# Kernel tuning notes

Measured on AMD Instinct MI355X. Metric: run time of the kernel, lower is better.

The kernel has to match this reference:

```python
import jax, jax.numpy as jnp
import numpy as np

B, C, H, W = 16, 64, 64, 64

def setup_inputs() -> dict:
    key = jax.random.key(0)
    k1, k2, k3, k4, k5 = jax.random.split(key, 5)
    x = jax.random.normal(k1, (B, C, H, W), dtype=jnp.float32)
    w1 = jax.random.normal(k2, (C // 2, C), dtype=jnp.float32) * (1.0 / np.sqrt(C))
    w2 = jax.random.normal(k3, (C // 2, C), dtype=jnp.float32) * (1.0 / np.sqrt(C))
    w3 = jax.random.normal(k4, (C, C), dtype=jnp.float32) * (1.0 / np.sqrt(C))
    gamma = jax.random.normal(k5, (1,), dtype=jnp.float32)
    return {"x": x, "w1": w1, "w2": w2, "w3": w3, "gamma": gamma}

def reference(x, w1, w2, w3, gamma):
    b, c, h, w = x.shape
    n = h * w
    xf = x.reshape(b, c, n)                      # [B, C, N] (1x1 conv == channel matmul)
    c1 = jnp.einsum('dc,bcn->bdn', w1, xf)       # [B, C/2, N]
    c2 = jnp.einsum('dc,bcn->bdn', w2, xf)       # [B, C/2, N]
    c3 = jnp.einsum('oc,bcn->bon', w3, xf)       # [B, C, N]
    # matrix[b,i,j] = sum_d c2[b,d,i] * c1[b,d,j]
    matrix = jnp.einsum('bdi,bdj->bij', c2, c1)  # [B, N, N]
    attention = jax.nn.softmax(matrix, axis=-1)  # softmax over last dim
    # refined[b,c,k] = sum_j c3[b,c,j] * attention[b,k,j]
    refined = jnp.einsum('bcj,bkj->bck', c3, attention)  # [B, C, N]
    refined = refined.reshape(b, c, h, w)
    return gamma[0] * refined + x
```

## Files before the change

kernel.cpp:

```cpp
#include <hip/hip_runtime.h>
#include <hip/hip_bf16.h>

#define Bn 16
#define Nn 4096
#define LOG2E 1.44269504088896f

#if __has_builtin(__builtin_amdgcn_exp2f)
#define EXP2(x) __builtin_amdgcn_exp2f(x)
#else
#define EXP2(x) __expf((x) * 0.69314718055994531f)
#endif

typedef __attribute__((ext_vector_type(8))) short bf16x8;
typedef __attribute__((ext_vector_type(16))) float f32x16;

static __device__ __forceinline__ unsigned short f2bf(float f) {
    union { float f; unsigned int u; } v; v.f = f;
    return (unsigned short)((v.u + 0x7fffu + ((v.u >> 16) & 1u)) >> 16);
}
static __device__ __forceinline__ int cvtpk(float lo, float hi) {
    int d; asm("v_cvt_pk_bf16_f32 %0, %1, %2" : "=v"(d) : "v"(lo), "v"(hi)); return d;
}
static __device__ __forceinline__ bf16x8 mkfrag(int a, int b, int c, int d) {
    union { int i[4]; bf16x8 v; } u; u.i[0]=a; u.i[1]=b; u.i[2]=c; u.i[3]=d; return u.v;
}

__global__ __launch_bounds__(256) void qkv_kernel(
    const float* __restrict__ x,
    const float* __restrict__ w1,
    const float* __restrict__ w2,
    const float* __restrict__ w3,
    uint4* __restrict__ Qf,
    uint4* __restrict__ Kf,
    uint4* __restrict__ Vf)
{
    __shared__ float wlds[128 * 64];
    __shared__ __align__(16) unsigned short vtile[64][136];

    const int t = threadIdx.x;
    {
        float4* wd = (float4*)wlds;
        const float4* s1 = (const float4*)w1;
        const float4* s2 = (const float4*)w2;
        const float4* s3 = (const float4*)w3;
        wd[t]       = s1[t];
        wd[256 + t] = s1[256 + t];
        wd[512 + t] = s2[t];
        wd[768 + t] = s2[256 + t];
        #pragma unroll
        for (int k = 0; k < 4; ++k) wd[1024 + k * 256 + t] = s3[k * 256 + t];
    }

    const int half = t >> 7;
    const int nl = t & 127;
    const int b = blockIdx.x >> 5;
    const int n = ((blockIdx.x & 31) << 7) + nl;
    const float* xb = x + ((size_t)b << 18) + n;
    float xr[64];
    #pragma unroll
    for (int c = 0; c < 64; ++c) xr[c] = xb[(size_t)c << 12];

    __syncthreads();

    if (half == 0) {
        const int ntile = ((blockIdx.x & 31) << 2) + (nl >> 5);
        #pragma unroll
        for (int sel = 0; sel < 2; ++sel) {
            const float* wbase = wlds + sel * 2048;
            const float scl = sel ? 1.0f : LOG2E;
            uint4* dst = (sel ? Qf : Kf) + (((size_t)b * 128 + ntile) * 2) * 64;
            #pragma unroll
            for (int dt = 0; dt < 2; ++dt) {
                float acc[16];
                #pragma unroll
                for (int i = 0; i < 16; ++i) {
                    const float* wr = wbase + (dt * 16 + i) * 64;
                    float a = 0.f;
                    #pragma unroll
                    for (int c4 = 0; c4 < 16; ++c4) {
                        const float4 wv = *(const float4*)(wr + c4 * 4);
                        a = fmaf(wv.x, xr[c4 * 4 + 0], a);
                        a = fmaf(wv.y, xr[c4 * 4 + 1], a);
                        a = fmaf(wv.z, xr[c4 * 4 + 2], a);
                        a = fmaf(wv.w, xr[c4 * 4 + 3], a);
                    }
                    acc[i] = a * scl;
                }
                uint4 u0, u1;
                u0.x = (unsigned)f2bf(acc[0])  | ((unsigned)f2bf(acc[1])  << 16);
                u0.y = (unsigned)f2bf(acc[2])  | ((unsigned)f2bf(acc[3])  << 16);
                u0.z = (unsigned)f2bf(acc[4])  | ((unsigned)f2bf(acc[5])  << 16);
                u0.w = (unsigned)f2bf(acc[6])  | ((unsigned)f2bf(acc[7])  << 16);
                u1.x = (unsigned)f2bf(acc[8])  | ((unsigned)f2bf(acc[9])  << 16);
                u1.y = (unsigned)f2bf(acc[10]) | ((unsigned)f2bf(acc[11]) << 16);
                u1.z = (unsigned)f2bf(acc[12]) | ((unsigned)f2bf(acc[13]) << 16);
                u1.w = (unsigned)f2bf(acc[14]) | ((unsigned)f2bf(acc[15]) << 16);
                dst[(size_t)dt * 64 + (nl & 31)]      = u0;
                dst[(size_t)dt * 64 + 32 + (nl & 31)] = u1;
            }
        }
    } else {
        #pragma unroll
        for (int dg = 0; dg < 8; ++dg) {
            #pragma unroll
            for (int i = 0; i < 8; ++i) {
                const float* wr = wlds + (64 + dg * 8 + i) * 64;
                float a = 0.f;
                #pragma unroll
                for (int c4 = 0; c4 < 16; ++c4) {
                    const float4 wv = *(const float4*)(wr + c4 * 4);
                    a = fmaf(wv.x, xr[c4 * 4 + 0], a);
                    a = fmaf(wv.y, xr[c4 * 4 + 1], a);
                    a = fmaf(wv.z, xr[c4 * 4 + 2], a);
                    a = fmaf(wv.w, xr[c4 * 4 + 3], a);
                }
                vtile[dg * 8 + i][nl] = f2bf(a);
            }
        }
    }
    __syncthreads();

    #pragma unroll
    for (int i = 0; i < 4; ++i) {
        const int slot = t * 4 + i;
        const int l   = slot & 63;
        const int jt  = (slot >> 6) & 1;
        const int ct  = (slot >> 7) & 1;
        const int kvt = slot >> 8;
        const int row  = ct * 32 + (l & 31);
        const int base = kvt * 32 + jt * 16 + ((l >> 5) << 2);
        const uint2 lo = *(const uint2*)&vtile[row][base];
        const uint2 hi = *(const uint2*)&vtile[row][base + 8];
        const int kvtg = ((blockIdx.x & 31) << 2) + kvt;
        Vf[((((size_t)b * 128 + kvtg) * 2 + ct) * 2 + jt) * 64 + l] =
            make_uint4(lo.x, lo.y, hi.x, hi.y);
    }
}

__global__ __launch_bounds__(512) void attn_kernel(
    const bf16x8* __restrict__ Qf,
    const bf16x8* __restrict__ Kf,
    const bf16x8* __restrict__ Vf,
    const float* __restrict__ x,
    const float* __restrict__ gamma,
    float* __restrict__ out)
{
    __shared__ __align__(16) unsigned char kvbuf[2 * 12288];
    __shared__ float mgbuf[4 * 64 * 37];

    const int t    = threadIdx.x;
    const int lane = t & 63;
    const int wv   = t >> 6;
    const int id   = blockIdx.x;
    const int b    = 2 * (id & 7) + ((id >> 3) >> 5);
    const int qg   = (id >> 3) & 31;
    const int qt   = qg * 4 + (wv & 3);
    const int h    = wv >> 2;

    const bf16x8* Qp = Qf + ((size_t)(b * 128 + qt) * 2) * 64;
    const bf16x8  qf0 = Qp[lane];
    const bf16x8  qf1 = Qp[64 + lane];
    const bf16x8* Kp = Kf + (size_t)b * 128 * 2 * 64;
    const bf16x8* Vp = Vf + (size_t)b * 128 * 4 * 64;

    const bf16x8 ones = mkfrag(0x3F803F80, 0x3F803F80, 0x3F803F80, 0x3F803F80);

    const int s0  = (t >= 384);
    const int r0  = t - s0 * 384;
    const int sl0 = r0 >> 6;
    const int l0  = r0 & 63;
    const int dof0 = s0 * 12288 + r0 * 16;
    const bool two = (t < 256);
    const int r1  = t + 128;
    const int sl1 = r1 >> 6;
    const int l1  = t & 63;
    const int dof1 = 12288 + r1 * 16;

    const bf16x8* sp0 = (sl0 < 2)
        ? (Kp + ((size_t)(s0 * 64) * 2 + sl0) * 64 + l0)
        : (Vp + ((size_t)(s0 * 64) * 4 + (sl0 - 2)) * 64 + l0);
    const int str0 = (sl0 < 2) ? 128 : 256;
    const bf16x8* sp1 = Vp + ((size_t)64 * 4 + (sl1 - 2)) * 64 + l1;

    {
        *(uint4*)(kvbuf + dof0) = *(const uint4*)sp0;
        sp0 += str0;
        if (two) {
            *(uint4*)(kvbuf + dof1) = *(const uint4*)sp1;
            sp1 += 256;
        }
    }
    __syncthreads();

    f32x16 o0 = {}, o1 = {}, lsum = {};

    for (int i = 0; i < 64; ++i) {
        uint4 st0, st1;
        if (i < 63) {
            st0 = *(const uint4*)sp0; sp0 += str0;
            if (two) { st1 = *(const uint4*)sp1; sp1 += 256; }
        }

        const bf16x8* bc = (const bf16x8*)(kvbuf + h * 12288 + (i & 1) * 6144);
        const bf16x8 kf0 = bc[lane];
        const bf16x8 kf1 = bc[64 + lane];
        const bf16x8 v00 = bc[128 + lane];
        const bf16x8 v01 = bc[192 + lane];
        const bf16x8 v10 = bc[256 + lane];
        const bf16x8 v11 = bc[320 + lane];

        f32x16 s;
        {
            f32x16 z = {};
            __builtin_amdgcn_s_setprio(1);
            s = __builtin_amdgcn_mfma_f32_32x32x16_bf16(kf0, qf0, z, 0, 0, 0);
            s = __builtin_amdgcn_mfma_f32_32x32x16_bf16(kf1, qf1, s, 0, 0, 0);
            __builtin_amdgcn_s_setprio(0);
        }

        float p[16];
        #pragma unroll
        for (int j = 0; j < 16; ++j) p[j] = EXP2(s[j]);

        const bf16x8 pf0 = mkfrag(cvtpk(p[0],  p[1]),  cvtpk(p[2],  p[3]),
                                  cvtpk(p[4],  p[5]),  cvtpk(p[6],  p[7]));
        const bf16x8 pf1 = mkfrag(cvtpk(p[8],  p[9]),  cvtpk(p[10], p[11]),
                                  cvtpk(p[12], p[13]), cvtpk(p[14], p[15]));

        __builtin_amdgcn_s_setprio(1);
        o0 = __builtin_amdgcn_mfma_f32_32x32x16_bf16(v00, pf0, o0, 0, 0, 0);
        o0 = __builtin_amdgcn_mfma_f32_32x32x16_bf16(v01, pf1, o0, 0, 0, 0);
        o1 = __builtin_amdgcn_mfma_f32_32x32x16_bf16(v10, pf0, o1, 0, 0, 0);
        o1 = __builtin_amdgcn_mfma_f32_32x32x16_bf16(v11, pf1, o1, 0, 0, 0);
        lsum = __builtin_amdgcn_mfma_f32_32x32x16_bf16(ones, pf0, lsum, 0, 0, 0);
        lsum = __builtin_amdgcn_mfma_f32_32x32x16_bf16(ones, pf1, lsum, 0, 0, 0);
        __builtin_amdgcn_s_setprio(0);

        if (i < 63) {
            const int bo = ((i + 1) & 1) * 6144;
            *(uint4*)(kvbuf + dof0 + bo) = st0;
            if (two) *(uint4*)(kvbuf + dof1 + bo) = st1;
        }
        __syncthreads();
    }

    float lacc = lsum[0];

    if (wv >= 4) {
        float* mg = mgbuf + ((size_t)(wv - 4) * 64 + lane) * 37;
        #pragma unroll
        for (int j = 0; j < 16; ++j) { mg[j] = o0[j]; mg[16 + j] = o1[j]; }
        mg[32] = lacc;
    }
    __syncthreads();
    if (wv < 4) {
        const float* mg = mgbuf + ((size_t)wv * 64 + lane) * 37;
        #pragma unroll
        for (int j = 0; j < 16; ++j) { o0[j] += mg[j]; o1[j] += mg[16 + j]; }
        lacc += mg[32];

        const float g = gamma[0];
        const float rl = 1.0f / lacc;
        const int n = qt * 32 + (lane & 31);
        const int hi1 = lane >> 5;
        #pragma unroll
        for (int r = 0; r < 16; ++r) {
            const int c0r = (r & 3) + 8 * (r >> 2) + 4 * hi1;
            {
                const size_t idx = (((size_t)b * 64 + c0r) << 12) + n;
                out[idx] = g * o0[r] * rl + x[idx];
            }
            {
                const size_t idx = (((size_t)b * 64 + 32 + c0r) << 12) + n;
                out[idx] = g * o1[r] * rl + x[idx];
            }
        }
    }
}

extern "C" void kernel_launch(void* const* d_in, const int* in_sizes, int n_in,
                              void* d_out, int out_size, void* d_ws, size_t ws_size,
                              hipStream_t stream) {
    const float* x     = (const float*)d_in[0];
    const float* w1    = (const float*)d_in[1];
    const float* w2    = (const float*)d_in[2];
    const float* w3    = (const float*)d_in[3];
    const float* gamma = (const float*)d_in[4];
    float* out = (float*)d_out;

    uint4* Qf = (uint4*)d_ws;
    uint4* Kf = Qf + (size_t)Bn * 128 * 2 * 64;
    uint4* Vf = Kf + (size_t)Bn * 128 * 2 * 64;

    qkv_kernel<<<512, 256, 0, stream>>>(x, w1, w2, w3, Qf, Kf, Vf);
    attn_kernel<<<512, 512, 0, stream>>>((const bf16x8*)Qf, (const bf16x8*)Kf,
                                         (const bf16x8*)Vf, x, gamma, out);
}
```

Measured before the change: 110.9 us.

## Split attention KV range four ways per block with two query tiles

Each 512-thread block now handles two query tiles instead of four and splits the key/value sequence into four quarters instead of two, launching twice as many blocks. Staging loads cover four KV streams per iteration over 32 steps, and partial outputs are merged through shared memory (reusing the KV buffer) in two reduction rounds. The aim is more blocks for better CU occupancy and a shorter serial loop per block. The cost is more K/V traffic per query tile and extra merge synchronisation.

```diff
diff --git a/kernel.cpp b/kernel.cpp
--- a/kernel.cpp
+++ b/kernel.cpp
@@ -145,17 +145,17 @@
     const float* __restrict__ gamma,
     float* __restrict__ out)
 {
-    __shared__ __align__(16) unsigned char kvbuf[2 * 12288];
-    __shared__ float mgbuf[4 * 64 * 37];
+    __shared__ __align__(16) unsigned char kvbuf[4 * 2 * 6144];
 
     const int t    = threadIdx.x;
     const int lane = t & 63;
     const int wv   = t >> 6;
     const int id   = blockIdx.x;
-    const int b    = 2 * (id & 7) + ((id >> 3) >> 5);
-    const int qg   = (id >> 3) & 31;
-    const int qt   = qg * 4 + (wv & 3);
-    const int h    = wv >> 2;
+    const int b    = 2 * (id & 7) + ((id >> 3) >> 6);
+    const int qp   = (id >> 3) & 63;
+    const int q    = wv & 1;
+    const int kvq  = wv >> 1;
+    const int qt   = qp * 2 + q;
 
     const bf16x8* Qp = Qf + ((size_t)(b * 128 + qt) * 2) * 64;
     const bf16x8  qf0 = Qp[lane];
@@ -165,43 +165,40 @@
 
     const bf16x8 ones = mkfrag(0x3F803F80, 0x3F803F80, 0x3F803F80, 0x3F803F80);
 
-    const int s0  = (t >= 384);
-    const int r0  = t - s0 * 384;
-    const int sl0 = r0 >> 6;
-    const int l0  = r0 & 63;
-    const int dof0 = s0 * 12288 + r0 * 16;
-    const bool two = (t < 256);
-    const int r1  = t + 128;
-    const int sl1 = r1 >> 6;
-    const int l1  = t & 63;
-    const int dof1 = 12288 + r1 * 16;
-
-    const bf16x8* sp0 = (sl0 < 2)
-        ? (Kp + ((size_t)(s0 * 64) * 2 + sl0) * 64 + l0)
-        : (Vp + ((size_t)(s0 * 64) * 4 + (sl0 - 2)) * 64 + l0);
-    const int str0 = (sl0 < 2) ? 128 : 256;
-    const bf16x8* sp1 = Vp + ((size_t)64 * 4 + (sl1 - 2)) * 64 + l1;
-
-    {
-        *(uint4*)(kvbuf + dof0) = *(const uint4*)sp0;
-        sp0 += str0;
-        if (two) {
-            *(uint4*)(kvbuf + dof1) = *(const uint4*)sp1;
-            sp1 += 256;
-        }
+    const bf16x8* sp[3];
+    int strd[3], dof[3];
+    #pragma unroll
+    for (int k = 0; k < 3; ++k) {
+        const int c = t + k * 512;
+        const int s = c / 384;
+        const int r = c - s * 384;
+        const int slot = r >> 6;
+        const int ln = r & 63;
+        dof[k] = s * 12288 + r * 16;
+        if (slot < 2) { sp[k] = Kp + ((size_t)(s * 32) * 2 + slot) * 64 + ln;       strd[k] = 128; }
+        else          { sp[k] = Vp + ((size_t)(s * 32) * 4 + (slot - 2)) * 64 + ln; strd[k] = 256; }
+    }
+
+    #pragma unroll
+    for (int k = 0; k < 3; ++k) {
+        *(uint4*)(kvbuf + dof[k]) = *(const uint4*)sp[k];
+        sp[k] += strd[k];
     }
     __syncthreads();
 
     f32x16 o0 = {}, o1 = {}, lsum = {};
 
-    for (int i = 0; i < 64; ++i) {
-        uint4 st0, st1;
-        if (i < 63) {
-            st0 = *(const uint4*)sp0; sp0 += str0;
-            if (two) { st1 = *(const uint4*)sp1; sp1 += 256; }
-        }
-
-        const bf16x8* bc = (const bf16x8*)(kvbuf + h * 12288 + (i & 1) * 6144);
+    for (int i = 0; i < 32; ++i) {
+        uint4 st[3];
+        if (i < 31) {
+            #pragma unroll
+            for (int k = 0; k < 3; ++k) {
+                st[k] = *(const uint4*)sp[k];
+                sp[k] += strd[k];
+            }
+        }
+
+        const bf16x8* bc = (const bf16x8*)(kvbuf + kvq * 12288 + (i & 1) * 6144);
         const bf16x8 kf0 = bc[lane];
         const bf16x8 kf1 = bc[64 + lane];
         const bf16x8 v00 = bc[128 + lane];
@@ -236,25 +233,44 @@
         lsum = __builtin_amdgcn_mfma_f32_32x32x16_bf16(ones, pf1, lsum, 0, 0, 0);
         __builtin_amdgcn_s_setprio(0);
 
-        if (i < 63) {
+        if (i < 31) {
             const int bo = ((i + 1) & 1) * 6144;
-            *(uint4*)(kvbuf + dof0 + bo) = st0;
-            if (two) *(uint4*)(kvbuf + dof1 + bo) = st1;
+            #pragma unroll
+            for (int k = 0; k < 3; ++k)
+                *(uint4*)(kvbuf + dof[k] + bo) = st[k];
         }
         __syncthreads();
     }
 
     float lacc = lsum[0];
 
-    if (wv >= 4) {
-        float* mg = mgbuf + ((size_t)(wv - 4) * 64 + lane) * 37;
+    float* const mbase = (float*)kvbuf;
+    if (kvq == 1 || kvq == 2) {
+        float* mg = mbase + ((size_t)((kvq - 1) * 2 + q) * 64 + lane) * 33;
         #pragma unroll
         for (int j = 0; j < 16; ++j) { mg[j] = o0[j]; mg[16 + j] = o1[j]; }
         mg[32] = lacc;
     }
     __syncthreads();
-    if (wv < 4) {
-        const float* mg = mgbuf + ((size_t)wv * 64 + lane) * 37;
+    if (kvq == 0) {
+        #pragma unroll
+        for (int blk = 0; blk < 2; ++blk) {
+            const float* mg = mbase + ((size_t)(blk * 2 + q) * 64 + lane) * 33;
+            #pragma unroll
+            for (int j = 0; j < 16; ++j) { o0[j] += mg[j]; o1[j] += mg[16 + j]; }
+            lacc += mg[32];
+        }
+    }
+    __syncthreads();
+    if (kvq == 3) {
+        float* mg = mbase + ((size_t)q * 64 + lane) * 33;
+        #pragma unroll
+        for (int j = 0; j < 16; ++j) { mg[j] = o0[j]; mg[16 + j] = o1[j]; }
+        mg[32] = lacc;
+    }
+    __syncthreads();
+    if (kvq == 0) {
+        const float* mg = mbase + ((size_t)q * 64 + lane) * 33;
         #pragma unroll
         for (int j = 0; j < 16; ++j) { o0[j] += mg[j]; o1[j] += mg[16 + j]; }
         lacc += mg[32];
@@ -293,6 +309,6 @@
     uint4* Vf = Kf + (size_t)Bn * 128 * 2 * 64;
 
     qkv_kernel<<<512, 256, 0, stream>>>(x, w1, w2, w3, Qf, Kf, Vf);
-    attn_kernel<<<512, 512, 0, stream>>>((const bf16x8*)Qf, (const bf16x8*)Kf,
-                                         (const bf16x8*)Vf, x, gamma, out);
-}
+    attn_kernel<<<1024, 512, 0, stream>>>((const bf16x8*)Qf, (const bf16x8*)Kf,
+                                          (const bf16x8*)Vf, x, gamma, out);
+}
```

Result: slower. 239.8 us (+116.2%).

## Balance projection work across waves with two positions per thread

Applied to the files above, without the earlier changes.

The projection stage now gives each of the four waves 32 output rows (K, Q, or half of V) over two spatial positions per thread, replacing the split where half the threads computed K and Q and the other half computed V. Each LDS weight float4 load now feeds two FMAs, and x is streamed in 16-channel chunks rather than held as 64 registers. This removes the wave-level imbalance and halves LDS weight traffic per FMA, at the cost of 64 accumulator registers per thread.

```diff
diff --git a/kernel.cpp b/kernel.cpp
--- a/kernel.cpp
+++ b/kernel.cpp
@@ -51,71 +51,83 @@
         for (int k = 0; k < 4; ++k) wd[1024 + k * 256 + t] = s3[k * 256 + t];
     }
 
-    const int half = t >> 7;
-    const int nl = t & 127;
-    const int b = blockIdx.x >> 5;
-    const int n = ((blockIdx.x & 31) << 7) + nl;
-    const float* xb = x + ((size_t)b << 18) + n;
-    float xr[64];
+    const int lane = t & 63;
+    const int wvq  = t >> 6;
+    const int b    = blockIdx.x >> 5;
+    const int nb   = (blockIdx.x & 31) << 7;
+    const float* xb0 = x + ((size_t)b << 18) + nb + lane;
+    const float* xb1 = x + ((size_t)b << 18) + nb + 64 + lane;
+
+    const float* wbase = (wvq == 0) ? wlds
+                       : (wvq == 1) ? (wlds + 2048)
+                                    : (wlds + 4096 + (wvq - 2) * 32 * 64);
+    const float scl = (wvq == 0) ? LOG2E : 1.0f;
+
+    float acc0[32], acc1[32];
     #pragma unroll
-    for (int c = 0; c < 64; ++c) xr[c] = xb[(size_t)c << 12];
+    for (int i = 0; i < 32; ++i) { acc0[i] = 0.f; acc1[i] = 0.f; }
 
     __syncthreads();
 
-    if (half == 0) {
-        const int ntile = ((blockIdx.x & 31) << 2) + (nl >> 5);
-        #pragma unroll
-        for (int sel = 0; sel < 2; ++sel) {
-            const float* wbase = wlds + sel * 2048;
-            const float scl = sel ? 1.0f : LOG2E;
-            uint4* dst = (sel ? Qf : Kf) + (((size_t)b * 128 + ntile) * 2) * 64;
+    #pragma unroll 1
+    for (int ch = 0; ch < 4; ++ch) {
+        float xr0[16], xr1[16];
+        #pragma unroll
+        for (int c = 0; c < 16; ++c) {
+            xr0[c] = xb0[(size_t)(ch * 16 + c) << 12];
+            xr1[c] = xb1[(size_t)(ch * 16 + c) << 12];
+        }
+        #pragma unroll
+        for (int i = 0; i < 32; ++i) {
+            const float* wr = wbase + i * 64 + ch * 16;
+            float a0 = acc0[i], a1 = acc1[i];
+            #pragma unroll
+            for (int c4 = 0; c4 < 4; ++c4) {
+                const float4 wv = *(const float4*)(wr + c4 * 4);
+                a0 = fmaf(wv.x, xr0[c4 * 4 + 0], a0);
+                a1 = fmaf(wv.x, xr1[c4 * 4 + 0], a1);
+                a0 = fmaf(wv.y, xr0[c4 * 4 + 1], a0);
+                a1 = fmaf(wv.y, xr1[c4 * 4 + 1], a1);
+                a0 = fmaf(wv.z, xr0[c4 * 4 + 2], a0);
+                a1 = fmaf(wv.z, xr1[c4 * 4 + 2], a1);
+                a0 = fmaf(wv.w, xr0[c4 * 4 + 3], a0);
+                a1 = fmaf(wv.w, xr1[c4 * 4 + 3], a1);
+            }
+            acc0[i] = a0; acc1[i] = a1;
+        }
+    }
+    #pragma unroll
+    for (int i = 0; i < 32; ++i) { acc0[i] *= scl; acc1[i] *= scl; }
+
+    if (wvq < 2) {
+        uint4* dstb = wvq ? Qf : Kf;
+        #pragma unroll
+        for (int pp = 0; pp < 2; ++pp) {
+            const float* ac = pp ? acc1 : acc0;
+            const int pos = pp * 64 + lane;
+            const int ntile = ((blockIdx.x & 31) << 2) + (pos >> 5);
+            uint4* dst = dstb + (((size_t)b * 128 + ntile) * 2) * 64;
             #pragma unroll
             for (int dt = 0; dt < 2; ++dt) {
-                float acc[16];
-                #pragma unroll
-                for (int i = 0; i < 16; ++i) {
-                    const float* wr = wbase + (dt * 16 + i) * 64;
-                    float a = 0.f;
-                    #pragma unroll
-                    for (int c4 = 0; c4 < 16; ++c4) {
-                        const float4 wv = *(const float4*)(wr + c4 * 4);
-                        a = fmaf(wv.x, xr[c4 * 4 + 0], a);
-                        a = fmaf(wv.y, xr[c4 * 4 + 1], a);
-                        a = fmaf(wv.z, xr[c4 * 4 + 2], a);
-                        a = fmaf(wv.w, xr[c4 * 4 + 3], a);
-                    }
-                    acc[i] = a * scl;
-                }
                 uint4 u0, u1;
-                u0.x = (unsigned)f2bf(acc[0])  | ((unsigned)f2bf(acc[1])  << 16);
-                u0.y = (unsigned)f2bf(acc[2])  | ((unsigned)f2bf(acc[3])  << 16);
-                u0.z = (unsigned)f2bf(acc[4])  | ((unsigned)f2bf(acc[5])  << 16);
-                u0.w = (unsigned)f2bf(acc[6])  | ((unsigned)f2bf(acc[7])  << 16);
-                u1.x = (unsigned)f2bf(acc[8])  | ((unsigned)f2bf(acc[9])  << 16);
-                u1.y = (unsigned)f2bf(acc[10]) | ((unsigned)f2bf(acc[11]) << 16);
-                u1.z = (unsigned)f2bf(acc[12]) | ((unsigned)f2bf(acc[13]) << 16);
-                u1.w = (unsigned)f2bf(acc[14]) | ((unsigned)f2bf(acc[15]) << 16);
-                dst[(size_t)dt * 64 + (nl & 31)]      = u0;
-                dst[(size_t)dt * 64 + 32 + (nl & 31)] = u1;
+                u0.x = (unsigned)f2bf(ac[dt*16+0])  | ((unsigned)f2bf(ac[dt*16+1])  << 16);
+                u0.y = (unsigned)f2bf(ac[dt*16+2])  | ((unsigned)f2bf(ac[dt*16+3])  << 16);
+                u0.z = (unsigned)f2bf(ac[dt*16+4])  | ((unsigned)f2bf(ac[dt*16+5])  << 16);
+                u0.w = (unsigned)f2bf(ac[dt*16+6])  | ((unsigned)f2bf(ac[dt*16+7])  << 16);
+                u1.x = (unsigned)f2bf(ac[dt*16+8])  | ((unsigned)f2bf(ac[dt*16+9])  << 16);
+                u1.y = (unsigned)f2bf(ac[dt*16+10]) | ((unsigned)f2bf(ac[dt*16+11]) << 16);
+                u1.z = (unsigned)f2bf(ac[dt*16+12]) | ((unsigned)f2bf(ac[dt*16+13]) << 16);
+                u1.w = (unsigned)f2bf(ac[dt*16+14]) | ((unsigned)f2bf(ac[dt*16+15]) << 16);
+                dst[(size_t)dt * 64 + (pos & 31)]      = u0;
+                dst[(size_t)dt * 64 + 32 + (pos & 31)] = u1;
             }
         }
     } else {
-        #pragma unroll
-        for (int dg = 0; dg < 8; ++dg) {
-            #pragma unroll
-            for (int i = 0; i < 8; ++i) {
-                const float* wr = wlds + (64 + dg * 8 + i) * 64;
-                float a = 0.f;
-                #pragma unroll
-                for (int c4 = 0; c4 < 16; ++c4) {
-                    const float4 wv = *(const float4*)(wr + c4 * 4);
-                    a = fmaf(wv.x, xr[c4 * 4 + 0], a);
-                    a = fmaf(wv.y, xr[c4 * 4 + 1], a);
-                    a = fmaf(wv.z, xr[c4 * 4 + 2], a);
-                    a = fmaf(wv.w, xr[c4 * 4 + 3], a);
-                }
-                vtile[dg * 8 + i][nl] = f2bf(a);
-            }
+        const int rbase = (wvq - 2) * 32;
+        #pragma unroll
+        for (int i = 0; i < 32; ++i) {
+            vtile[rbase + i][lane]      = f2bf(acc0[i]);
+            vtile[rbase + i][64 + lane] = f2bf(acc1[i]);
         }
     }
     __syncthreads();
```

Result: faster. 101.0 us (-9.0%).
